# Kernel optimization log

Hardware: AMD Instinct MI355X
Metric: run time of the kernel (lower is better)

The kernel has to match this reference:

```python
import jax, jax.numpy as jnp
import numpy as np

N, IN, H, OUT, C = 1024, 64, 64, 64, 32
EPS = 1e-5   # SAKELayer.epsilon
INF = 1e5    # SAKELayer.inf


def _w(key, i, o, scale=1.0):
    return jax.random.normal(key, (i, o), jnp.float32) * (scale / np.sqrt(i))


def setup_inputs() -> dict:
    key = jax.random.key(0)
    ks = jax.random.split(key, 16)
    return dict(
        h=jax.random.normal(ks[0], (N, IN), jnp.float32),
        x=jax.random.normal(ks[1], (N, 3), jnp.float32),
        # edge model (ConcatenationFilter): Linear(2*IN+1,H), SiLU, Linear(H,H)
        ew1=_w(ks[2], 2 * IN + 1, H), eb1=jnp.zeros((H,), jnp.float32),
        ew2=_w(ks[3], H, H), eb2=jnp.zeros((H,), jnp.float32),
        # node_mlp: Linear(2H+IN,H), SiLU, Linear(H,OUT)
        nw1=_w(ks[4], 2 * H + IN, H), nb1=jnp.zeros((H,), jnp.float32),
        nw2=_w(ks[5], H, OUT), nb2=jnp.zeros((OUT,), jnp.float32),
        # coordinate_mlp: Linear(H,H), SiLU, Linear(H,1,bias=False) xavier gain 1e-3
        cw1=_w(ks[6], H, H), cb1=jnp.zeros((H,), jnp.float32),
        cw2=_w(ks[7], H, 1, scale=1e-3),
        # semantic_attention_mlp: Linear(H,1), LeakyReLU
        aw=_w(ks[8], H, 1), ab=jnp.zeros((1,), jnp.float32),
        # coefficients_mlp: Linear(H,H), SiLU, Linear(H,C)
        fw1=_w(ks[9], H, H), fb1=jnp.zeros((H,), jnp.float32),
        fw2=_w(ks[10], H, C), fb2=jnp.zeros((C,), jnp.float32),
        # post_norm_mlp: Linear(C,H), SiLU, Linear(H,H)
        pw1=_w(ks[11], C, H), pb1=jnp.zeros((H,), jnp.float32),
        pw2=_w(ks[12], H, H), pb2=jnp.zeros((H,), jnp.float32),
        log_gamma=jnp.array(0.0, jnp.float32),
    )


def reference(h, x, ew1, eb1, ew2, eb2, nw1, nb1, nw2, nb2, cw1, cb1, cw2,
              aw, ab, fw1, fb1, fw2, fb2, pw1, pb1, pw2, pb2, log_gamma):
    n, d_in = h.shape
    silu = jax.nn.silu
    eye = jnp.eye(n, dtype=h.dtype)[:, :, None]                    # [n,n,1]

    x_minus_xt = x[:, None, :] - x[None, :, :]                     # [n,n,3]
    norm = jnp.sqrt(jnp.sum(x_minus_xt ** 2, -1, keepdims=True) + EPS)  # [n,n,1]

    h_cat_ht = jnp.concatenate(
        [jnp.broadcast_to(h[:, None, :], (n, n, d_in)),
         jnp.broadcast_to(h[None, :, :], (n, n, d_in))], -1)       # [n,n,2*IN]

    # edge model: MLP over concat(features, distance)
    e_in = jnp.concatenate([h_cat_ht, norm], -1)                   # [n,n,2*IN+1]
    h_e = silu(e_in @ ew1 + eb1) @ ew2 + eb2                       # [n,n,H]

    # euclidean attention over neighbors j (diag masked by +INF distance)
    att_e = jax.nn.softmax(-(norm + INF * eye) * jnp.exp(log_gamma), axis=1)
    # semantic attention
    att_s = jax.nn.softmax(jax.nn.leaky_relu(h_e @ aw + ab) - INF * eye, axis=1)
    comb = att_e * att_s
    comb = comb / (jnp.sum(comb, axis=1, keepdims=True) + EPS)     # [n,n,1]
    h_e_att = h_e * comb                                           # [n,n,H]

    # spatial attention: equivariant coefficient combinations
    coeff = silu(h_e_att @ fw1 + fb1) @ fw2 + fb2                  # [n,n,C]
    dirs = x_minus_xt / (norm + 1.0)                               # [n,n,3]
    combos = jnp.einsum('ijc,ijd->icd', coeff, dirs) / n           # mean over j -> [n,C,3]
    h_comb = silu(jnp.sum(combos ** 2, -1) @ pw1 + pb1) @ pw2 + pb2  # [n,H]

    # node update
    h_agg = jnp.sum(h_e_att, axis=1)                               # [n,H]
    node_in = jnp.concatenate([h, h_agg, h_comb], -1)              # [n,2H+IN]
    h_out = h + (silu(node_in @ nw1 + nb1) @ nw2 + nb2)            # residual

    # equivariant coordinate update
    phi = silu(h_e @ cw1 + cb1) @ cw2                              # [n,n,1]
    x_out = x + jnp.mean(x_minus_xt * phi, axis=1)                 # [n,3]
    return h_out, x_out
```

## Files before the change

kernel.cpp:

```cpp
#include <hip/hip_runtime.h>
#include <hip/hip_bf16.h>

#define NN 1024
#define LSTR 72
#define EPSV 1e-5f
#define BIGINF 1e5f

typedef __attribute__((ext_vector_type(8))) short short8;
typedef __attribute__((ext_vector_type(4))) short short4v;
typedef __attribute__((ext_vector_type(4))) float f32x4;

__device__ __forceinline__ float siluf(float v) {
    return v * __builtin_amdgcn_rcpf(1.0f + __expf(-v));
}
__device__ __forceinline__ float pnorm(float dx, float dy, float dz) {
    return sqrtf(dx * dx + dy * dy + dz * dz + EPSV);
}
__device__ __forceinline__ float wsum(float v) {
#pragma unroll
    for (int off = 32; off > 0; off >>= 1) v += __shfl_xor(v, off, 64);
    return v;
}
__device__ __forceinline__ float redquad(float v) {
    v += __shfl_xor(v, 16, 64); v += __shfl_xor(v, 32, 64);
    return v;
}
__device__ __forceinline__ short f2bs(float v) {
    __hip_bfloat16 b = __float2bfloat16(v);
    return *reinterpret_cast<short*>(&b);
}
__device__ __forceinline__ short f2bt(float v) {
    return (short)(__float_as_uint(v) >> 16);
}

__global__ void kA(const float* __restrict__ h, const float* __restrict__ ew1,
                   const float* __restrict__ eb1, const float* __restrict__ ew2,
                   const float* __restrict__ cw1, const float* __restrict__ fw1,
                   const float* __restrict__ fw2, const float* __restrict__ aw,
                   const float* __restrict__ ab, const float* __restrict__ eb2,
                   float* __restrict__ HA, float* __restrict__ HB,
                   float* __restrict__ HBT, short* __restrict__ ew2T,
                   short* __restrict__ cw1T, short* __restrict__ fw1T,
                   short* __restrict__ fw2T, float* __restrict__ wsv,
                   float* __restrict__ svb) {
    const int b = blockIdx.x;
    const int o = threadIdx.x;
    if (b < NN) {
        const int i = b;
        float hv = h[i * 64 + o];
        float a = 0.f, bb = eb1[o];
#pragma unroll
        for (int k = 0; k < 64; k++) {
            float hk = __shfl(hv, k, 64);
            a += hk * ew1[k * 64 + o];
            bb += hk * ew1[(64 + k) * 64 + o];
        }
        HA[i * 64 + o] = a;
        HB[i * 64 + o] = bb;
        HBT[o * NN + i] = bb;
    } else if (b < NN + 64) {
        const int r = b - NN;
        ew2T[r * 64 + o] = f2bs(ew2[o * 64 + r]);
        cw1T[r * 64 + o] = f2bs(cw1[o * 64 + r]);
        fw1T[r * 64 + o] = f2bs(fw1[o * 64 + r]);
        if (r < 32) fw2T[r * 64 + o] = f2bs(fw2[o * 32 + r]);
    } else {
        float s = 0.f;
#pragma unroll
        for (int q = 0; q < 64; q++) s += ew2[o * 64 + q] * aw[q];
        wsv[o] = s;
        float e = wsum(eb2[o] * aw[o]);
        if (o == 0) svb[0] = e + ab[0];
    }
}

__global__ __launch_bounds__(256) void kBn(
    const float* __restrict__ x, const float* __restrict__ ew1,
    const float* __restrict__ HA, const float* __restrict__ HBT,
    const float* __restrict__ wsv, const float* __restrict__ svb,
    const float* __restrict__ lg, float* __restrict__ ls,
    float* __restrict__ rowm, float* __restrict__ rowd) {
    const int i = blockIdx.x;
    const int t = threadIdx.x;
    const float* HAi = HA + i * 64;
    const float* w1 = ew1 + 128 * 64;
    const float gamma = __expf(lg[0]);
    const float svb0 = svb[0];
    const float xi0 = x[i * 3 + 0], xi1 = x[i * 3 + 1], xi2 = x[i * 3 + 2];

    float4 xa = ((const float4*)x)[3 * t + 0];
    float4 xb = ((const float4*)x)[3 * t + 1];
    float4 xc = ((const float4*)x)[3 * t + 2];
    float nrm[4], le[4], lv[4];
    {
        float dx0 = xi0 - xa.x, dy0 = xi1 - xa.y, dz0 = xi2 - xa.z;
        float dx1 = xi0 - xa.w, dy1 = xi1 - xb.x, dz1 = xi2 - xb.y;
        float dx2 = xi0 - xb.z, dy2 = xi1 - xb.w, dz2 = xi2 - xc.x;
        float dx3 = xi0 - xc.y, dy3 = xi1 - xc.z, dz3 = xi2 - xc.w;
        nrm[0] = pnorm(dx0, dy0, dz0);
        nrm[1] = pnorm(dx1, dy1, dz1);
        nrm[2] = pnorm(dx2, dy2, dz2);
        nrm[3] = pnorm(dx3, dy3, dz3);
    }
    float d0 = 0.f, d1 = 0.f, d2 = 0.f, d3 = 0.f;
#pragma unroll 8
    for (int k = 0; k < 64; k++) {
        float4 hb = *(const float4*)&HBT[k * NN + 4 * t];
        float hk = HAi[k], w1k = w1[k], wv = wsv[k];
        d0 += siluf(hk + hb.x + nrm[0] * w1k) * wv;
        d1 += siluf(hk + hb.y + nrm[1] * w1k) * wv;
        d2 += siluf(hk + hb.z + nrm[2] * w1k) * wv;
        d3 += siluf(hk + hb.w + nrm[3] * w1k) * wv;
    }
    float me = -3.0e38f, ms = -3.0e38f;
    float4 svo;
    {
        float dd[4] = {d0, d1, d2, d3};
#pragma unroll
        for (int m = 0; m < 4; m++) {
            int j = 4 * t + m;
            float sv = dd[m] + svb0;
            sv = sv >= 0.f ? sv : 0.01f * sv;
            if (j == i) sv -= BIGINF;
            lv[m] = sv;
            le[m] = -(nrm[m] + (j == i ? BIGINF : 0.f)) * gamma;
            me = fmaxf(me, le[m]);
            ms = fmaxf(ms, lv[m]);
        }
        svo.x = lv[0]; svo.y = lv[1]; svo.z = lv[2]; svo.w = lv[3];
    }
    *(float4*)&ls[(size_t)i * NN + 4 * t] = svo;

    __shared__ float sm[4], ss[4], s1[4], s2[4], s3[4];
#pragma unroll
    for (int off = 32; off > 0; off >>= 1) {
        me = fmaxf(me, __shfl_xor(me, off, 64));
        ms = fmaxf(ms, __shfl_xor(ms, off, 64));
    }
    const int w = t >> 6;
    if ((t & 63) == 0) { sm[w] = me; ss[w] = ms; }
    __syncthreads();
    me = fmaxf(fmaxf(sm[0], sm[1]), fmaxf(sm[2], sm[3]));
    ms = fmaxf(fmaxf(ss[0], ss[1]), fmaxf(ss[2], ss[3]));
    float Se = 0.f, Ss = 0.f, Sq = 0.f;
#pragma unroll
    for (int m = 0; m < 4; m++) {
        float ee = __expf(le[m] - me);
        float es = __expf(lv[m] - ms);
        Se += ee; Ss += es; Sq += ee * es;
    }
    Se = wsum(Se); Ss = wsum(Ss); Sq = wsum(Sq);
    if ((t & 63) == 0) { s1[w] = Se; s2[w] = Ss; s3[w] = Sq; }
    __syncthreads();
    if (t == 0) {
        rowm[i] = me + ms;
        rowd[i] = (s3[0] + s3[1] + s3[2] + s3[3]) +
                  EPSV * (s1[0] + s1[1] + s1[2] + s1[3]) * (s2[0] + s2[1] + s2[2] + s2[3]);
    }
}

__device__ __forceinline__ void stageW(const short* __restrict__ g, short* s,
                                       int tid, int rows) {
    for (int c = tid; c < rows * 16; c += 512) {
        int r = c >> 4, q = c & 15;
        *(short4v*)&s[r * LSTR + q * 4] = *(const short4v*)&g[r * 64 + q * 4];
    }
}

__global__ __launch_bounds__(512) void kD(
    const float* __restrict__ x, const float* __restrict__ ew1,
    const float* __restrict__ eb2, const float* __restrict__ cb1,
    const float* __restrict__ fb1, const float* __restrict__ lg,
    const float* __restrict__ fw2, const float* __restrict__ fb2,
    const float* __restrict__ cw2,
    const float* __restrict__ HA, const float* __restrict__ HB,
    const short* __restrict__ ew2T, const short* __restrict__ cw1T,
    const short* __restrict__ fw1T,
    const float* __restrict__ ls, const float* __restrict__ rowm,
    const float* __restrict__ rowd, float* __restrict__ hagg,
    float* __restrict__ combos, float* __restrict__ xupd) {
    __shared__ __align__(16) short sWe[64 * LSTR];
    __shared__ __align__(16) short sWf[64 * LSTR];
    __shared__ __align__(16) short sWc[64 * LSTR];
    __shared__ __align__(16) short sScr[8][16 * LSTR];
    __shared__ float sHag[64], sG[192], sH2[192], sSd[3];

    const int tid = threadIdx.x;
    const int i = blockIdx.x;
    const int lane = tid & 63, w = tid >> 6;
    const int col = lane & 15, quad = lane >> 4;

    stageW(ew2T, sWe, tid, 64);
    stageW(fw1T, sWf, tid, 64);
    stageW(cw1T, sWc, tid, 64);
    if (tid < 64) sHag[tid] = 0.f;
    else if (tid < 256) sG[tid - 64] = 0.f;
    else if (tid < 448) sH2[tid - 256] = 0.f;
    else if (tid < 451) sSd[tid - 448] = 0.f;

    short* scr = sScr[w];
    const float gamma = __expf(lg[0]);

    float eb[4], cbv[4], fbv[4];
#pragma unroll
    for (int nb = 0; nb < 4; nb++) {
        eb[nb] = eb2[nb * 16 + col];
        cbv[nb] = cb1[nb * 16 + col];
        fbv[nb] = fb1[nb * 16 + col];
    }
    const float rm = rowm[i];
    const float invd = 1.0f / rowd[i];
    const float xi0 = x[i * 3 + 0], xi1 = x[i * 3 + 1], xi2 = x[i * 3 + 2];
    const float* lsi = ls + (size_t)i * NN;

    float hagA[4] = {0.f, 0.f, 0.f, 0.f};
    float Ga[12]  = {0.f, 0.f, 0.f, 0.f, 0.f, 0.f, 0.f, 0.f, 0.f, 0.f, 0.f, 0.f};
    float H2a[12] = {0.f, 0.f, 0.f, 0.f, 0.f, 0.f, 0.f, 0.f, 0.f, 0.f, 0.f, 0.f};
    float sdx = 0.f, sdy = 0.f, sdz = 0.f;
    __syncthreads();

#pragma unroll 1
    for (int jt = 0; jt < 8; jt++) {
        const int r = jt * 128 + w * 16 + col;
        float dx = xi0 - x[r * 3 + 0], dy = xi1 - x[r * 3 + 1], dz = xi2 - x[r * 3 + 2];
        float nr = pnorm(dx, dy, dz);
        float iv = __builtin_amdgcn_rcpf(nr + 1.0f);
        sdx += dx * iv; sdy += dy * iv; sdz += dz * iv;
        float le = -(nr + (r == i ? BIGINF : 0.f)) * gamma;
        float cb = __expf(le + lsi[r] - rm) * invd;

        short8 af[2];
#pragma unroll
        for (int kb = 0; kb < 2; kb++) {
            const float* hA = &HA[i * 64 + kb * 32 + quad * 8];
            const float* wr = &ew1[128 * 64 + kb * 32 + quad * 8];
            const float* hb = &HB[r * 64 + kb * 32 + quad * 8];
#pragma unroll
            for (int t = 0; t < 8; t++)
                af[kb][t] = f2bt(siluf(hA[t] + hb[t] + nr * wr[t]));
        }
        f32x4 ac[4] = {{0.f,0.f,0.f,0.f},{0.f,0.f,0.f,0.f},{0.f,0.f,0.f,0.f},{0.f,0.f,0.f,0.f}};
#pragma unroll
        for (int kb = 0; kb < 2; kb++) {
#pragma unroll
            for (int nb = 0; nb < 4; nb++) {
                short8 b = *(const short8*)&sWe[(nb * 16 + col) * LSTR + kb * 32 + quad * 8];
                ac[nb] = __builtin_amdgcn_mfma_f32_16x16x32_bf16(af[kb], b, ac[nb], 0, 0, 0);
            }
        }
        float cm[4];
#pragma unroll
        for (int reg = 0; reg < 4; reg++) cm[reg] = __shfl(cb, quad * 4 + reg, 64);
#pragma unroll
        for (int nb = 0; nb < 4; nb++) {
#pragma unroll
            for (int reg = 0; reg < 4; reg++) {
                float h0 = ac[nb][reg] + eb[nb];
                scr[(quad * 4 + reg) * LSTR + nb * 16 + col] = f2bt(h0);
                hagA[nb] += h0 * cm[reg];
            }
        }
        short8 a0 = *(const short8*)&scr[col * LSTR + quad * 8];
        short8 a1 = *(const short8*)&scr[col * LSTR + 32 + quad * 8];

        {
            f32x4 p[4] = {{0.f,0.f,0.f,0.f},{0.f,0.f,0.f,0.f},{0.f,0.f,0.f,0.f},{0.f,0.f,0.f,0.f}};
#pragma unroll
            for (int nb = 0; nb < 4; nb++) {
                short8 b0 = *(const short8*)&sWc[(nb * 16 + col) * LSTR + quad * 8];
                short8 b1 = *(const short8*)&sWc[(nb * 16 + col) * LSTR + 32 + quad * 8];
                p[nb] = __builtin_amdgcn_mfma_f32_16x16x32_bf16(a0, b0, p[nb], 0, 0, 0);
                p[nb] = __builtin_amdgcn_mfma_f32_16x16x32_bf16(a1, b1, p[nb], 0, 0, 0);
            }
#pragma unroll
            for (int reg = 0; reg < 4; reg++) {
                int sl = quad * 4 + reg;
                float tx = __shfl(dx, sl, 64), ty = __shfl(dy, sl, 64), tz = __shfl(dz, sl, 64);
#pragma unroll
                for (int nb = 0; nb < 4; nb++) {
                    float s0 = siluf(p[nb][reg] + cbv[nb]);
                    H2a[nb * 3 + 0] += s0 * tx;
                    H2a[nb * 3 + 1] += s0 * ty;
                    H2a[nb * 3 + 2] += s0 * tz;
                }
            }
        }

        {
            f32x4 v[4] = {{0.f,0.f,0.f,0.f},{0.f,0.f,0.f,0.f},{0.f,0.f,0.f,0.f},{0.f,0.f,0.f,0.f}};
#pragma unroll
            for (int nb = 0; nb < 4; nb++) {
                short8 b0 = *(const short8*)&sWf[(nb * 16 + col) * LSTR + quad * 8];
                short8 b1 = *(const short8*)&sWf[(nb * 16 + col) * LSTR + 32 + quad * 8];
                v[nb] = __builtin_amdgcn_mfma_f32_16x16x32_bf16(a0, b0, v[nb], 0, 0, 0);
                v[nb] = __builtin_amdgcn_mfma_f32_16x16x32_bf16(a1, b1, v[nb], 0, 0, 0);
            }
#pragma unroll
            for (int reg = 0; reg < 4; reg++) {
                int sl = quad * 4 + reg;
                float ti = __shfl(iv, sl, 64);
                float fx = __shfl(dx, sl, 64) * ti;
                float fy = __shfl(dy, sl, 64) * ti;
                float fz = __shfl(dz, sl, 64) * ti;
#pragma unroll
                for (int nb = 0; nb < 4; nb++) {
                    float w0 = siluf(cm[reg] * v[nb][reg] + fbv[nb]);
                    Ga[nb * 3 + 0] += w0 * fx;
                    Ga[nb * 3 + 1] += w0 * fy;
                    Ga[nb * 3 + 2] += w0 * fz;
                }
            }
        }
    }

#pragma unroll
    for (int nb = 0; nb < 4; nb++) {
        float v = redquad(hagA[nb]);
        if (quad == 0) atomicAdd(&sHag[nb * 16 + col], v);
    }
#pragma unroll
    for (int nb = 0; nb < 4; nb++) {
#pragma unroll
        for (int d = 0; d < 3; d++) {
            float v = redquad(H2a[nb * 3 + d]);
            if (quad == 0) atomicAdd(&sH2[(nb * 16 + col) * 3 + d], v);
            float g = redquad(Ga[nb * 3 + d]);
            if (quad == 0) atomicAdd(&sG[(nb * 16 + col) * 3 + d], g);
        }
    }
    sdx = wsum(sdx); sdy = wsum(sdy); sdz = wsum(sdz);
    if (lane == 0) {
        atomicAdd(&sSd[0], 0.25f * sdx);
        atomicAdd(&sSd[1], 0.25f * sdy);
        atomicAdd(&sSd[2], 0.25f * sdz);
    }
    __syncthreads();

    if (tid < 128) {
        int c = tid >> 2, d = tid & 3;
        if (d < 3) {
            float acc = fb2[c] * sSd[d];
#pragma unroll
            for (int m = 0; m < 64; m++) acc += fw2[m * 32 + c] * sG[m * 3 + d];
            combos[i * 96 + c * 3 + d] = acc;
        }
    } else if (tid < 131) {
        int d = tid - 128;
        float acc = 0.f;
#pragma unroll
        for (int n = 0; n < 64; n++) acc += cw2[n] * sH2[n * 3 + d];
        xupd[i * 3 + d] = acc;
    } else if (tid >= 192 && tid < 256) {
        hagg[i * 64 + tid - 192] = sHag[tid - 192];
    }
}

__global__ void kE(const float* __restrict__ h, const float* __restrict__ x,
                   const float* __restrict__ nw1, const float* __restrict__ nb1,
                   const float* __restrict__ nw2, const float* __restrict__ nb2,
                   const float* __restrict__ pw1, const float* __restrict__ pb1,
                   const float* __restrict__ pw2, const float* __restrict__ pb2,
                   const float* __restrict__ hagg, const float* __restrict__ combos,
                   const float* __restrict__ xupd, float* __restrict__ out) {
    const int i = blockIdx.x, o = threadIdx.x;
    const float invN = 1.0f / (float)NN;
    float r = 0.f;
    if (o < 32) {
        float v0 = combos[i * 96 + o * 3 + 0] * invN;
        float v1 = combos[i * 96 + o * 3 + 1] * invN;
        float v2 = combos[i * 96 + o * 3 + 2] * invN;
        r = v0 * v0 + v1 * v1 + v2 * v2;
    }
    float t1 = pb1[o];
#pragma unroll
    for (int k = 0; k < 32; k++) t1 += __shfl(r, k, 64) * pw1[k * 64 + o];
    t1 = siluf(t1);
    float hc = pb2[o];
#pragma unroll
    for (int k = 0; k < 64; k++) hc += __shfl(t1, k, 64) * pw2[k * 64 + o];
    float hi = h[i * 64 + o];
    float ha = hagg[i * 64 + o];
    float t2 = nb1[o];
#pragma unroll
    for (int k = 0; k < 64; k++) t2 += __shfl(hi, k, 64) * nw1[k * 64 + o];
#pragma unroll
    for (int k = 0; k < 64; k++) t2 += __shfl(ha, k, 64) * nw1[(64 + k) * 64 + o];
#pragma unroll
    for (int k = 0; k < 64; k++) t2 += __shfl(hc, k, 64) * nw1[(128 + k) * 64 + o];
    t2 = siluf(t2);
    float ho = hi + nb2[o];
#pragma unroll
    for (int k = 0; k < 64; k++) ho += __shfl(t2, k, 64) * nw2[k * 64 + o];
    out[i * 64 + o] = ho;
    if (o < 3)
        out[NN * 64 + i * 3 + o] = x[i * 3 + o] + xupd[i * 3 + o] * invN;
}

extern "C" void kernel_launch(void* const* d_in, const int* in_sizes, int n_in,
                              void* d_out, int out_size, void* d_ws, size_t ws_size,
                              hipStream_t stream) {
    (void)in_sizes; (void)n_in; (void)out_size; (void)ws_size;
    const float* h   = (const float*)d_in[0];
    const float* x   = (const float*)d_in[1];
    const float* ew1 = (const float*)d_in[2];
    const float* eb1 = (const float*)d_in[3];
    const float* ew2 = (const float*)d_in[4];
    const float* eb2 = (const float*)d_in[5];
    const float* nw1 = (const float*)d_in[6];
    const float* nb1 = (const float*)d_in[7];
    const float* nw2 = (const float*)d_in[8];
    const float* nb2 = (const float*)d_in[9];
    const float* cw1 = (const float*)d_in[10];
    const float* cb1 = (const float*)d_in[11];
    const float* cw2 = (const float*)d_in[12];
    const float* aw  = (const float*)d_in[13];
    const float* ab  = (const float*)d_in[14];
    const float* fw1 = (const float*)d_in[15];
    const float* fb1 = (const float*)d_in[16];
    const float* fw2 = (const float*)d_in[17];
    const float* fb2 = (const float*)d_in[18];
    const float* pw1 = (const float*)d_in[19];
    const float* pb1 = (const float*)d_in[20];
    const float* pw2 = (const float*)d_in[21];
    const float* pb2 = (const float*)d_in[22];
    const float* lg  = (const float*)d_in[23];
    float* out = (float*)d_out;

    float* W      = (float*)d_ws;
    float* ls     = W;
    float* HA     = ls + (size_t)NN * NN;
    float* HB     = HA + NN * 64;
    float* HBT    = HB + NN * 64;
    float* rowm   = HBT + NN * 64;
    float* rowd   = rowm + NN;
    float* hagg   = rowd + NN;
    float* combos = hagg + NN * 64;
    float* xupd   = combos + NN * 96;
    float* wsv    = xupd + NN * 3;
    float* svb    = wsv + 64;
    short* ew2T   = (short*)(svb + 4);
    short* cw1T   = ew2T + 64 * 64;
    short* fw1T   = cw1T + 64 * 64;
    short* fw2T   = fw1T + 64 * 64;

    kA<<<NN + 65, 64, 0, stream>>>(h, ew1, eb1, ew2, cw1, fw1, fw2, aw, ab, eb2,
                                   HA, HB, HBT, ew2T, cw1T, fw1T, fw2T, wsv, svb);
    kBn<<<NN, 256, 0, stream>>>(x, ew1, HA, HBT, wsv, svb, lg, ls, rowm, rowd);
    kD<<<NN, 512, 0, stream>>>(x, ew1, eb2, cb1, fb1, lg, fw2, fb2, cw2,
                               HA, HB, ew2T, cw1T, fw1T, ls, rowm, rowd,
                               hagg, combos, xupd);
    kE<<<NN, 64, 0, stream>>>(h, x, nw1, nb1, nw2, nb2, pw1, pb1, pw2, pb2,
                              hagg, combos, xupd, out);
}
```

Before: 257.7 us.

## Fuse attention-stat kernel into edge kernel, caching first-layer activations in LDS

Merges the row softmax statistics pass into the main per-row edge kernel. The first edge-MLP layer's SiLU activations for all 1024 neighbours are computed once, stored as bf16 in a ~158KB LDS buffer, and reused as MFMA A-operands instead of being recomputed. This removes the global logit round-trip and one launch. Weight B-operands are now read from global/L1 rather than staged in LDS. The big LDS footprint limits each CU to one 512-thread block, which may reduce latency hiding.

```diff
diff --git a/kernel.cpp b/kernel.cpp
--- a/kernel.cpp
+++ b/kernel.cpp
@@ -3,6 +3,7 @@
 
 #define NN 1024
 #define LSTR 72
+#define USTR 68
 #define EPSV 1e-5f
 #define BIGINF 1e5f
 
@@ -19,6 +20,11 @@
 __device__ __forceinline__ float wsum(float v) {
 #pragma unroll
     for (int off = 32; off > 0; off >>= 1) v += __shfl_xor(v, off, 64);
+    return v;
+}
+__device__ __forceinline__ float wmax(float v) {
+#pragma unroll
+    for (int off = 32; off > 0; off >>= 1) v = fmaxf(v, __shfl_xor(v, off, 64));
     return v;
 }
 __device__ __forceinline__ float redquad(float v) {
@@ -74,133 +80,97 @@
     }
 }
 
-__global__ __launch_bounds__(256) void kBn(
-    const float* __restrict__ x, const float* __restrict__ ew1,
-    const float* __restrict__ HA, const float* __restrict__ HBT,
-    const float* __restrict__ wsv, const float* __restrict__ svb,
-    const float* __restrict__ lg, float* __restrict__ ls,
-    float* __restrict__ rowm, float* __restrict__ rowd) {
-    const int i = blockIdx.x;
-    const int t = threadIdx.x;
-    const float* HAi = HA + i * 64;
-    const float* w1 = ew1 + 128 * 64;
-    const float gamma = __expf(lg[0]);
-    const float svb0 = svb[0];
-    const float xi0 = x[i * 3 + 0], xi1 = x[i * 3 + 1], xi2 = x[i * 3 + 2];
-
-    float4 xa = ((const float4*)x)[3 * t + 0];
-    float4 xb = ((const float4*)x)[3 * t + 1];
-    float4 xc = ((const float4*)x)[3 * t + 2];
-    float nrm[4], le[4], lv[4];
-    {
-        float dx0 = xi0 - xa.x, dy0 = xi1 - xa.y, dz0 = xi2 - xa.z;
-        float dx1 = xi0 - xa.w, dy1 = xi1 - xb.x, dz1 = xi2 - xb.y;
-        float dx2 = xi0 - xb.z, dy2 = xi1 - xb.w, dz2 = xi2 - xc.x;
-        float dx3 = xi0 - xc.y, dy3 = xi1 - xc.z, dz3 = xi2 - xc.w;
-        nrm[0] = pnorm(dx0, dy0, dz0);
-        nrm[1] = pnorm(dx1, dy1, dz1);
-        nrm[2] = pnorm(dx2, dy2, dz2);
-        nrm[3] = pnorm(dx3, dy3, dz3);
-    }
-    float d0 = 0.f, d1 = 0.f, d2 = 0.f, d3 = 0.f;
-#pragma unroll 8
-    for (int k = 0; k < 64; k++) {
-        float4 hb = *(const float4*)&HBT[k * NN + 4 * t];
-        float hk = HAi[k], w1k = w1[k], wv = wsv[k];
-        d0 += siluf(hk + hb.x + nrm[0] * w1k) * wv;
-        d1 += siluf(hk + hb.y + nrm[1] * w1k) * wv;
-        d2 += siluf(hk + hb.z + nrm[2] * w1k) * wv;
-        d3 += siluf(hk + hb.w + nrm[3] * w1k) * wv;
-    }
-    float me = -3.0e38f, ms = -3.0e38f;
-    float4 svo;
-    {
-        float dd[4] = {d0, d1, d2, d3};
-#pragma unroll
-        for (int m = 0; m < 4; m++) {
-            int j = 4 * t + m;
-            float sv = dd[m] + svb0;
-            sv = sv >= 0.f ? sv : 0.01f * sv;
-            if (j == i) sv -= BIGINF;
-            lv[m] = sv;
-            le[m] = -(nrm[m] + (j == i ? BIGINF : 0.f)) * gamma;
-            me = fmaxf(me, le[m]);
-            ms = fmaxf(ms, lv[m]);
-        }
-        svo.x = lv[0]; svo.y = lv[1]; svo.z = lv[2]; svo.w = lv[3];
-    }
-    *(float4*)&ls[(size_t)i * NN + 4 * t] = svo;
-
-    __shared__ float sm[4], ss[4], s1[4], s2[4], s3[4];
-#pragma unroll
-    for (int off = 32; off > 0; off >>= 1) {
-        me = fmaxf(me, __shfl_xor(me, off, 64));
-        ms = fmaxf(ms, __shfl_xor(ms, off, 64));
-    }
-    const int w = t >> 6;
-    if ((t & 63) == 0) { sm[w] = me; ss[w] = ms; }
-    __syncthreads();
-    me = fmaxf(fmaxf(sm[0], sm[1]), fmaxf(sm[2], sm[3]));
-    ms = fmaxf(fmaxf(ss[0], ss[1]), fmaxf(ss[2], ss[3]));
-    float Se = 0.f, Ss = 0.f, Sq = 0.f;
-#pragma unroll
-    for (int m = 0; m < 4; m++) {
-        float ee = __expf(le[m] - me);
-        float es = __expf(lv[m] - ms);
-        Se += ee; Ss += es; Sq += ee * es;
-    }
-    Se = wsum(Se); Ss = wsum(Ss); Sq = wsum(Sq);
-    if ((t & 63) == 0) { s1[w] = Se; s2[w] = Ss; s3[w] = Sq; }
-    __syncthreads();
-    if (t == 0) {
-        rowm[i] = me + ms;
-        rowd[i] = (s3[0] + s3[1] + s3[2] + s3[3]) +
-                  EPSV * (s1[0] + s1[1] + s1[2] + s1[3]) * (s2[0] + s2[1] + s2[2] + s2[3]);
-    }
-}
-
-__device__ __forceinline__ void stageW(const short* __restrict__ g, short* s,
-                                       int tid, int rows) {
-    for (int c = tid; c < rows * 16; c += 512) {
-        int r = c >> 4, q = c & 15;
-        *(short4v*)&s[r * LSTR + q * 4] = *(const short4v*)&g[r * 64 + q * 4];
-    }
-}
-
-__global__ __launch_bounds__(512) void kD(
+__global__ __launch_bounds__(512) void kF(
     const float* __restrict__ x, const float* __restrict__ ew1,
     const float* __restrict__ eb2, const float* __restrict__ cb1,
     const float* __restrict__ fb1, const float* __restrict__ lg,
     const float* __restrict__ fw2, const float* __restrict__ fb2,
     const float* __restrict__ cw2,
-    const float* __restrict__ HA, const float* __restrict__ HB,
+    const float* __restrict__ HA, const float* __restrict__ HBT,
     const short* __restrict__ ew2T, const short* __restrict__ cw1T,
     const short* __restrict__ fw1T,
-    const float* __restrict__ ls, const float* __restrict__ rowm,
-    const float* __restrict__ rowd, float* __restrict__ hagg,
-    float* __restrict__ combos, float* __restrict__ xupd) {
-    __shared__ __align__(16) short sWe[64 * LSTR];
-    __shared__ __align__(16) short sWf[64 * LSTR];
-    __shared__ __align__(16) short sWc[64 * LSTR];
-    __shared__ __align__(16) short sScr[8][16 * LSTR];
-    __shared__ float sHag[64], sG[192], sH2[192], sSd[3];
+    const float* __restrict__ wsv, const float* __restrict__ svb,
+    float* __restrict__ hagg, float* __restrict__ combos,
+    float* __restrict__ xupd) {
+    __shared__ __align__(16) char smem[161792];
+    short* sU = (short*)smem;
+    short* scrB = (short*)(smem + 139264);
+    float* sLv = (float*)(smem + 157696);
+    float* sRm = (float*)(smem + 139264);
+    float* sRs = sRm + 8;
+    float* sR1 = sRm + 16;
+    float* sR2 = sRm + 24;
+    float* sR3 = sRm + 32;
+    float* sHag = (float*)(smem + 139264);
+    float* sG = sHag + 64;
+    float* sH2 = sG + 192;
+    float* sSd = sH2 + 192;
 
     const int tid = threadIdx.x;
     const int i = blockIdx.x;
     const int lane = tid & 63, w = tid >> 6;
     const int col = lane & 15, quad = lane >> 4;
 
-    stageW(ew2T, sWe, tid, 64);
-    stageW(fw1T, sWf, tid, 64);
-    stageW(cw1T, sWc, tid, 64);
-    if (tid < 64) sHag[tid] = 0.f;
-    else if (tid < 256) sG[tid - 64] = 0.f;
-    else if (tid < 448) sH2[tid - 256] = 0.f;
-    else if (tid < 451) sSd[tid - 448] = 0.f;
-
-    short* scr = sScr[w];
     const float gamma = __expf(lg[0]);
-
+    const float svb0 = svb[0];
+    const float xi0 = x[i * 3 + 0], xi1 = x[i * 3 + 1], xi2 = x[i * 3 + 2];
+    const float* HAi = HA + i * 64;
+    const float* w1 = ew1 + 128 * 64;
+
+    float lvv[2], lev[2];
+    float meT = -3.0e38f, msT = -3.0e38f;
+#pragma unroll
+    for (int it = 0; it < 2; it++) {
+        const int j = it * 512 + tid;
+        float dx = xi0 - x[j * 3 + 0], dy = xi1 - x[j * 3 + 1], dz = xi2 - x[j * 3 + 2];
+        float nr = pnorm(dx, dy, dz);
+        float d = 0.f;
+        short* urow = &sU[j * USTR];
+#pragma unroll 4
+        for (int k0 = 0; k0 < 64; k0 += 4) {
+            short4v pk;
+#pragma unroll
+            for (int q = 0; q < 4; q++) {
+                int k = k0 + q;
+                float u = siluf(HAi[k] + HBT[(size_t)k * NN + j] + nr * w1[k]);
+                d += u * wsv[k];
+                pk[q] = f2bt(u);
+            }
+            *(short4v*)&urow[k0] = pk;
+        }
+        float sv = d + svb0;
+        sv = sv >= 0.f ? sv : 0.01f * sv;
+        float le = -(nr + (j == i ? BIGINF : 0.f)) * gamma;
+        if (j == i) sv -= BIGINF;
+        lvv[it] = sv; lev[it] = le;
+        sLv[j] = sv;
+        meT = fmaxf(meT, le); msT = fmaxf(msT, sv);
+    }
+    meT = wmax(meT); msT = wmax(msT);
+    if (lane == 0) { sRm[w] = meT; sRs[w] = msT; }
+    __syncthreads();
+    float me = sRm[0], ms = sRs[0];
+#pragma unroll
+    for (int q = 1; q < 8; q++) { me = fmaxf(me, sRm[q]); ms = fmaxf(ms, sRs[q]); }
+    float Se = 0.f, Ss = 0.f, Sq = 0.f;
+#pragma unroll
+    for (int it = 0; it < 2; it++) {
+        float ee = __expf(lev[it] - me);
+        float es = __expf(lvv[it] - ms);
+        Se += ee; Ss += es; Sq += ee * es;
+    }
+    Se = wsum(Se); Ss = wsum(Ss); Sq = wsum(Sq);
+    __syncthreads();
+    if (lane == 0) { sR1[w] = Se; sR2[w] = Ss; sR3[w] = Sq; }
+    __syncthreads();
+    float tSe = 0.f, tSs = 0.f, tSq = 0.f;
+#pragma unroll
+    for (int q = 0; q < 8; q++) { tSe += sR1[q]; tSs += sR2[q]; tSq += sR3[q]; }
+    const float rm = me + ms;
+    const float invd = 1.0f / (tSq + EPSV * tSe * tSs);
+    __syncthreads();
+
+    short* scr = scrB + w * 16 * LSTR;
     float eb[4], cbv[4], fbv[4];
 #pragma unroll
     for (int nb = 0; nb < 4; nb++) {
@@ -208,16 +178,10 @@
         cbv[nb] = cb1[nb * 16 + col];
         fbv[nb] = fb1[nb * 16 + col];
     }
-    const float rm = rowm[i];
-    const float invd = 1.0f / rowd[i];
-    const float xi0 = x[i * 3 + 0], xi1 = x[i * 3 + 1], xi2 = x[i * 3 + 2];
-    const float* lsi = ls + (size_t)i * NN;
-
     float hagA[4] = {0.f, 0.f, 0.f, 0.f};
     float Ga[12]  = {0.f, 0.f, 0.f, 0.f, 0.f, 0.f, 0.f, 0.f, 0.f, 0.f, 0.f, 0.f};
     float H2a[12] = {0.f, 0.f, 0.f, 0.f, 0.f, 0.f, 0.f, 0.f, 0.f, 0.f, 0.f, 0.f};
     float sdx = 0.f, sdy = 0.f, sdz = 0.f;
-    __syncthreads();
 
 #pragma unroll 1
     for (int jt = 0; jt < 8; jt++) {
@@ -227,24 +191,21 @@
         float iv = __builtin_amdgcn_rcpf(nr + 1.0f);
         sdx += dx * iv; sdy += dy * iv; sdz += dz * iv;
         float le = -(nr + (r == i ? BIGINF : 0.f)) * gamma;
-        float cb = __expf(le + lsi[r] - rm) * invd;
+        float cb = __expf(le + sLv[r] - rm) * invd;
 
         short8 af[2];
 #pragma unroll
         for (int kb = 0; kb < 2; kb++) {
-            const float* hA = &HA[i * 64 + kb * 32 + quad * 8];
-            const float* wr = &ew1[128 * 64 + kb * 32 + quad * 8];
-            const float* hb = &HB[r * 64 + kb * 32 + quad * 8];
-#pragma unroll
-            for (int t = 0; t < 8; t++)
-                af[kb][t] = f2bt(siluf(hA[t] + hb[t] + nr * wr[t]));
+            short4v u0 = *(const short4v*)&sU[r * USTR + kb * 32 + quad * 8];
+            short4v u1 = *(const short4v*)&sU[r * USTR + kb * 32 + quad * 8 + 4];
+            af[kb] = __builtin_shufflevector(u0, u1, 0, 1, 2, 3, 4, 5, 6, 7);
         }
         f32x4 ac[4] = {{0.f,0.f,0.f,0.f},{0.f,0.f,0.f,0.f},{0.f,0.f,0.f,0.f},{0.f,0.f,0.f,0.f}};
 #pragma unroll
         for (int kb = 0; kb < 2; kb++) {
 #pragma unroll
             for (int nb = 0; nb < 4; nb++) {
-                short8 b = *(const short8*)&sWe[(nb * 16 + col) * LSTR + kb * 32 + quad * 8];
+                short8 b = *(const short8*)&ew2T[(nb * 16 + col) * 64 + kb * 32 + quad * 8];
                 ac[nb] = __builtin_amdgcn_mfma_f32_16x16x32_bf16(af[kb], b, ac[nb], 0, 0, 0);
             }
         }
@@ -267,8 +228,8 @@
             f32x4 p[4] = {{0.f,0.f,0.f,0.f},{0.f,0.f,0.f,0.f},{0.f,0.f,0.f,0.f},{0.f,0.f,0.f,0.f}};
 #pragma unroll
             for (int nb = 0; nb < 4; nb++) {
-                short8 b0 = *(const short8*)&sWc[(nb * 16 + col) * LSTR + quad * 8];
-                short8 b1 = *(const short8*)&sWc[(nb * 16 + col) * LSTR + 32 + quad * 8];
+                short8 b0 = *(const short8*)&cw1T[(nb * 16 + col) * 64 + quad * 8];
+                short8 b1 = *(const short8*)&cw1T[(nb * 16 + col) * 64 + 32 + quad * 8];
                 p[nb] = __builtin_amdgcn_mfma_f32_16x16x32_bf16(a0, b0, p[nb], 0, 0, 0);
                 p[nb] = __builtin_amdgcn_mfma_f32_16x16x32_bf16(a1, b1, p[nb], 0, 0, 0);
             }
@@ -285,13 +246,12 @@
                 }
             }
         }
-
         {
             f32x4 v[4] = {{0.f,0.f,0.f,0.f},{0.f,0.f,0.f,0.f},{0.f,0.f,0.f,0.f},{0.f,0.f,0.f,0.f}};
 #pragma unroll
             for (int nb = 0; nb < 4; nb++) {
-                short8 b0 = *(const short8*)&sWf[(nb * 16 + col) * LSTR + quad * 8];
-                short8 b1 = *(const short8*)&sWf[(nb * 16 + col) * LSTR + 32 + quad * 8];
+                short8 b0 = *(const short8*)&fw1T[(nb * 16 + col) * 64 + quad * 8];
+                short8 b1 = *(const short8*)&fw1T[(nb * 16 + col) * 64 + 32 + quad * 8];
                 v[nb] = __builtin_amdgcn_mfma_f32_16x16x32_bf16(a0, b0, v[nb], 0, 0, 0);
                 v[nb] = __builtin_amdgcn_mfma_f32_16x16x32_bf16(a1, b1, v[nb], 0, 0, 0);
             }
@@ -313,6 +273,9 @@
         }
     }
 
+    __syncthreads();
+    for (int c = tid; c < 452; c += 512) sHag[c] = 0.f;
+    __syncthreads();
 #pragma unroll
     for (int nb = 0; nb < 4; nb++) {
         float v = redquad(hagA[nb]);
@@ -335,7 +298,6 @@
         atomicAdd(&sSd[2], 0.25f * sdz);
     }
     __syncthreads();
-
     if (tid < 128) {
         int c = tid >> 2, d = tid & 3;
         if (d < 3) {
@@ -445,9 +407,8 @@
 
     kA<<<NN + 65, 64, 0, stream>>>(h, ew1, eb1, ew2, cw1, fw1, fw2, aw, ab, eb2,
                                    HA, HB, HBT, ew2T, cw1T, fw1T, fw2T, wsv, svb);
-    kBn<<<NN, 256, 0, stream>>>(x, ew1, HA, HBT, wsv, svb, lg, ls, rowm, rowd);
-    kD<<<NN, 512, 0, stream>>>(x, ew1, eb2, cb1, fb1, lg, fw2, fb2, cw2,
-                               HA, HB, ew2T, cw1T, fw1T, ls, rowm, rowd,
+    kF<<<NN, 512, 0, stream>>>(x, ew1, eb2, cb1, fb1, lg, fw2, fb2, cw2,
+                               HA, HBT, ew2T, cw1T, fw1T, wsv, svb,
                                hagg, combos, xupd);
     kE<<<NN, 64, 0, stream>>>(h, x, nw1, nb1, nw2, nb2, pw1, pb1, pw2, pb2,
                               hagg, combos, xupd, out);
```

Measured after the change: 301.4 us. 1.17x slower.
